# Kernel optimization log

Hardware: AMD Instinct MI355X
Metric: run time of the kernel (lower is better)

Reference implementation:

```python
import jax, jax.numpy as jnp
import numpy as np

N, E, G = 100000, 1600000, 8
IN, H, OUT = 3, 64, 20


def setup_inputs() -> dict:
    key = jax.random.key(0)
    ks = jax.random.split(key, 24)
    def nrm(k, shape, scale=0.1):
        return jax.random.normal(k, shape, dtype=jnp.float32) * scale
    inp = {}
    inp["x"] = jax.random.normal(ks[0], (N, IN), dtype=jnp.float32)
    inp["edge_index"] = jax.random.randint(ks[1], (2, E), 0, N, dtype=jnp.int32)
    inp["batch"] = jnp.sort(jax.random.randint(ks[2], (N,), 0, G, dtype=jnp.int32))
    dims = [(IN, H), (H, H), (H, H)]  # 3 GATConv layers (initial + layers-1)
    for i, (di, do) in enumerate(dims):
        inp[f"W{i}"] = nrm(ks[3 + 4 * i], (di, do))
        inp[f"as{i}"] = nrm(ks[4 + 4 * i], (do,))
        inp[f"ad{i}"] = nrm(ks[5 + 4 * i], (do,))
        inp[f"b{i}"] = jnp.zeros((do,), jnp.float32)
    inp["vn_emb0"] = jnp.zeros((1, H), jnp.float32)  # constant-0 init per module
    inp["m1_w1"] = nrm(ks[15], (H, H)); inp["m1_b1"] = jnp.zeros((H,), jnp.float32)
    inp["m1_w2"] = nrm(ks[16], (H, H)); inp["m1_b2"] = jnp.zeros((H,), jnp.float32)
    inp["mf_w1"] = nrm(ks[17], (H, H)); inp["mf_b1"] = jnp.zeros((H,), jnp.float32)
    inp["mf_w2"] = nrm(ks[18], (H, OUT)); inp["mf_b2"] = jnp.zeros((OUT,), jnp.float32)
    inp["out_w"] = nrm(ks[19], (H, OUT)); inp["out_b"] = jnp.zeros((OUT,), jnp.float32)
    return inp


def _gat(x, src, dst, W, a_s, a_d, b):
    # PyG GATConv, 1 head: h = xW; e_ij = LeakyReLU_0.2(a_s.h_j + a_d.h_i);
    # alpha = softmax over incoming edges of each dst node; out_i = sum_j alpha_ij h_j + b
    h = x @ W                                                  # [N, H]
    lg = jax.nn.leaky_relu((h @ a_s)[src] + (h @ a_d)[dst], 0.2)  # [E+N]
    m = jax.ops.segment_max(lg, dst, num_segments=N)
    m = jnp.where(jnp.isfinite(m), m, 0.0)
    p = jnp.exp(lg - m[dst])
    denom = jax.ops.segment_sum(p, dst, num_segments=N)
    alpha = p / denom[dst]
    return jax.ops.segment_sum(alpha[:, None] * h[src], dst, num_segments=N) + b


def _forward(x, edge_index, batch, params):
    (W0, as0, ad0, b0, W1, as1, ad1, b1, W2, as2, ad2, b2,
     vn_emb0, m1_w1, m1_b1, m1_w2, m1_b2, mf_w1, mf_b1, mf_w2, mf_b2,
     out_w, out_b) = params
    loops = jnp.arange(N, dtype=edge_index.dtype)  # GATConv add_self_loops=True
    src = jnp.concatenate([edge_index[0], loops])
    dst = jnp.concatenate([edge_index[1], loops])
    act = lambda v: jax.nn.leaky_relu(v, 0.01)  # nn.LeakyReLU default slope
    h = act(_gat(x, src, dst, W0, as0, ad0, b0))
    h = act(_gat(h, src, dst, W1, as1, ad1, b1))
    h = act(_gat(h, src, dst, W2, as2, ad2, b2))
    # virtual node: global_add_pool(out, batch) + Embedding(0) (zero-init)
    vn = jax.ops.segment_sum(h, batch, num_segments=G) + vn_emb0[0]
    vn = jax.nn.relu(vn @ m1_w1 + m1_b1)
    vn = jax.nn.relu(vn @ m1_w2 + m1_b2)
    vn = jax.nn.relu(vn @ mf_w1 + mf_b1)
    vn = jax.nn.relu(vn @ mf_w2 + mf_b2)
    return (h @ out_w + out_b, vn)


def reference(x, edge_index, batch, W0, as0, ad0, b0, W1, as1, ad1, b1,
              W2, as2, ad2, b2, vn_emb0, m1_w1, m1_b1, m1_w2, m1_b2,
              mf_w1, mf_b1, mf_w2, mf_b2, out_w, out_b):
    params = (W0, as0, ad0, b0, W1, as1, ad1, b1, W2, as2, ad2, b2,
              vn_emb0, m1_w1, m1_b1, m1_w2, m1_b2, mf_w1, mf_b1, mf_w2, mf_b2,
              out_w, out_b)
    return _forward(x, edge_index, batch, params)
```

## Files before the change

kernel.cpp:

```cpp
#include <hip/hip_runtime.h>
#include <hip/hip_bf16.h>

#define H 64
#define OUTD 20
#define NGRAPH 8
#define NBK 256
#define CAPB 8192
#define MAXDEG 63

typedef __attribute__((ext_vector_type(8))) short bf16x8;
typedef __attribute__((ext_vector_type(4))) float f32x4;
typedef __attribute__((ext_vector_type(8))) unsigned short u16x8;


__device__ __forceinline__ float ldp(const void* p, int i, bool f32) {
    return f32 ? ((const float*)p)[i]
               : __bfloat162float(((const __hip_bfloat16*)p)[i]);
}

__device__ __forceinline__ float bfu(unsigned short u) {
    union { unsigned int i; float f; } c; c.i = ((unsigned)u) << 16; return c.f;
}
__device__ __forceinline__ unsigned short fbits(float f) {
    __hip_bfloat16 b = __float2bfloat16(f);
    return *reinterpret_cast<unsigned short*>(&b);
}

__global__ void detect_dtype(const unsigned short* __restrict__ xb, int n_u16,
                             int* __restrict__ flag) {
    __shared__ int sh[256];
    int t = threadIdx.x;
    int m = min(n_u16, 4096);
    int bad = 0;
    for (int i = t; i < m; i += 256) {
        unsigned e = (xb[i] >> 7) & 0xFF;
        bad += (e >= 0x90) ? 1 : 0;
    }
    sh[t] = bad;
    __syncthreads();
    for (int off = 128; off; off >>= 1) {
        if (t < off) sh[t] += sh[t + off];
        __syncthreads();
    }
    if (t == 0) *flag = (sh[0] > (m >> 4)) ? 1 : 0;
}

__device__ __forceinline__ void ew_node(const float* __restrict__ s, float di,
                                        unsigned* __restrict__ cb,
                                        int deg, int node, int n, int l) {
    int D = deg + 1;
    int dm1 = deg;
    int e0 = l, e1 = l + 16, e2 = l + 32, e3 = l + 48;
    unsigned p0 = cb[min(e0, dm1)];
    unsigned p1 = cb[min(e1, dm1)];
    unsigned p2 = cb[min(e2, dm1)];
    unsigned p3 = cb[min(e3, dm1)];
    int j0 = (e0 < deg) ? (int)(p0 >> 15) : node;
    int j1 = (e1 < deg) ? (int)(p1 >> 15) : node;
    int j2 = (e2 < deg) ? (int)(p2 >> 15) : node;
    int j3 = (e3 < deg) ? (int)(p3 >> 15) : node;
    if ((unsigned)j0 >= (unsigned)n) j0 = 0;
    if ((unsigned)j1 >= (unsigned)n) j1 = 0;
    if ((unsigned)j2 >= (unsigned)n) j2 = 0;
    if ((unsigned)j3 >= (unsigned)n) j3 = 0;
    float v0 = s[j0] + di, v1 = s[j1] + di, v2 = s[j2] + di, v3 = s[j3] + di;
    v0 = v0 > 0.f ? v0 : 0.2f * v0;
    v1 = v1 > 0.f ? v1 : 0.2f * v1;
    v2 = v2 > 0.f ? v2 : 0.2f * v2;
    v3 = v3 > 0.f ? v3 : 0.2f * v3;
    bool m0 = e0 < D, m1 = e1 < D, m2 = e2 < D, m3 = e3 < D;
    float a0 = m0 ? v0 : -INFINITY, a1 = m1 ? v1 : -INFINITY;
    float a2 = m2 ? v2 : -INFINITY, a3 = m3 ? v3 : -INFINITY;
    float mx = fmaxf(fmaxf(a0, a1), fmaxf(a2, a3));
    for (int o = 1; o < 16; o <<= 1) mx = fmaxf(mx, __shfl_xor(mx, o));
    float x0 = m0 ? __expf(v0 - mx) : 0.f;
    float x1 = m1 ? __expf(v1 - mx) : 0.f;
    float x2 = m2 ? __expf(v2 - mx) : 0.f;
    float x3 = m3 ? __expf(v3 - mx) : 0.f;
    float ws = x0 + x1 + x2 + x3;
    for (int o = 1; o < 16; o <<= 1) ws += __shfl_xor(ws, o);
    float inv = 1.f / fmaxf(ws, 1e-20f);
    if (m0) cb[e0] = ((unsigned)j0 << 15) |
                     (((__float_as_uint(x0 * inv) + 0x8000u) >> 16) & 0x7FFFu);
    if (m1) cb[e1] = ((unsigned)j1 << 15) |
                     (((__float_as_uint(x1 * inv) + 0x8000u) >> 16) & 0x7FFFu);
    if (m2) cb[e2] = ((unsigned)j2 << 15) |
                     (((__float_as_uint(x2 * inv) + 0x8000u) >> 16) & 0x7FFFu);
    if (m3) cb[e3] = ((unsigned)j3 << 15) |
                     (((__float_as_uint(x3 * inv) + 0x8000u) >> 16) & 0x7FFFu);
}

__global__ void fillC_dense0(const int* __restrict__ src, const int* __restrict__ dst,
                             int* __restrict__ gcur, unsigned* __restrict__ ebuf,
                             int E, int n, int nC, int EPC, int nbk,
                             const void* __restrict__ x, const void* __restrict__ W,
                             const void* __restrict__ a_s, const void* __restrict__ a_d,
                             __hip_bfloat16* __restrict__ h, float* __restrict__ s,
                             float* __restrict__ d, const int* __restrict__ flagp) {
    if ((int)blockIdx.x < nC) {
        __shared__ unsigned lcnt[NBK];
        __shared__ int lbase[NBK];
        int t = threadIdx.x;
        for (int i = t; i < NBK; i += 256) lcnt[i] = 0;
        __syncthreads();
        int base = blockIdx.x * (256 * EPC) + t;
        for (int i = 0; i < EPC; ++i) {
            int e = base + i * 256;
            if (e < E) {
                int dn = dst[e];
                if ((unsigned)dn < (unsigned)n) atomicAdd(&lcnt[dn >> 9], 1u);
            }
        }
        __syncthreads();
        for (int i = t; i < nbk; i += 256) {
            unsigned c = lcnt[i];
            lbase[i] = c ? atomicAdd(&gcur[i], (int)c) : 0;
            lcnt[i] = 0;
        }
        __syncthreads();
        for (int i = 0; i < EPC; ++i) {
            int e = base + i * 256;
            if (e < E) {
                int dn = dst[e];
                if ((unsigned)dn < (unsigned)n) {
                    int b = dn >> 9;
                    unsigned pos = (unsigned)lbase[b] + atomicAdd(&lcnt[b], 1u);
                    if (pos < CAPB)
                        ebuf[(size_t)b * CAPB + pos] =
                            ((unsigned)src[e] << 9) | (unsigned)(dn & 511);
                }
            }
        }
        return;
    }
    const bool f32 = (*flagp != 0);
    int idx = ((int)blockIdx.x - nC) * 256 + threadIdx.x;
    int node = idx >> 6;
    int f = idx & 63;
    if (node >= n) return;
    float acc = 0.f;
    for (int k = 0; k < 3; ++k)
        acc += ldp(x, node * 3 + k, f32) * ldp(W, k * H + f, f32);
    ((short*)h)[((size_t)(f >> 5) * n + node) * 32 + (f & 31)] = (short)fbits(acc);
    float sv = acc * ldp(a_s, f, f32);
    float dv = acc * ldp(a_d, f, f32);
    for (int off = 32; off; off >>= 1) {
        sv += __shfl_xor(sv, off);
        dv += __shfl_xor(dv, off);
    }
    if (f == 0) { s[node] = sv; d[node] = dv; }
}

__global__ __launch_bounds__(512) void bucketD(const unsigned* __restrict__ ebuf,
                                               const int* __restrict__ gcur,
                                               unsigned* __restrict__ cntoff,
                                               unsigned* __restrict__ col,
                                               int* __restrict__ gtot, int n,
                                               const float* __restrict__ s,
                                               const float* __restrict__ d) {
    __shared__ unsigned lcnt[512];
    __shared__ int loff[512];
    __shared__ int sc[512];
    __shared__ int sdeg[512];
    __shared__ int sbase;
    int b = blockIdx.x, t = threadIdx.x;
    lcnt[t] = 0;
    __syncthreads();
    int end = min(gcur[b], CAPB);
    const unsigned* reg = ebuf + (size_t)b * CAPB;
    for (int i = t; i < end; i += 512) atomicAdd(&lcnt[reg[i] & 511u], 1u);
    __syncthreads();
    int node = (b << 9) + t;
    int degc = (node < n) ? (int)min(lcnt[t], (unsigned)MAXDEG) : -1;
    int slots = degc + 1;
    sc[t] = slots;
    __syncthreads();
    for (int ofs = 1; ofs < 512; ofs <<= 1) {
        int v = (t >= ofs) ? sc[t - ofs] : 0;
        __syncthreads();
        sc[t] += v;
        __syncthreads();
    }
    if (t == 511) sbase = atomicAdd(gtot, sc[511]);
    __syncthreads();
    int myoff = sbase + sc[t] - slots;
    int dg = (degc > 0) ? degc : 0;
    loff[t] = myoff;
    sdeg[t] = dg;
    if (node < n) cntoff[node] = (unsigned)myoff | ((unsigned)dg << 24);
    lcnt[t] = 0;
    __syncthreads();
    for (int i = t; i < end; i += 512) {
        unsigned e = reg[i];
        int loc = (int)(e & 511u);
        unsigned pos = atomicAdd(&lcnt[loc], 1u);
        if ((int)pos < sdeg[loc])
            col[loff[loc] + pos] = (e >> 9) << 15;
    }
    __syncthreads();
    int l = t & 15;
    int base16 = t >> 4;
    for (int it = 0; it < 16; ++it) {
        int local = base16 + 32 * it;
        int nd = (b << 9) + local;
        if (nd < n)
            ew_node(s, d[nd], col + loff[local], sdeg[local], nd, n, l);
    }
}

__global__ void edge_weights(const float* __restrict__ s, const float* __restrict__ d,
                             const unsigned* __restrict__ cntoff,
                             unsigned* __restrict__ col, int n) {
    int node = ((int)blockIdx.x * 256 + (int)threadIdx.x) >> 4;
    if (node >= n) return;
    unsigned co = cntoff[node];
    ew_node(s, d[node], col + (co & 0xFFFFFFu), (int)(co >> 24), node, n,
            threadIdx.x & 15);
}

#define ACC8(w, hv) { \
    a[0] += w * bfu(hv[0]); a[1] += w * bfu(hv[1]); \
    a[2] += w * bfu(hv[2]); a[3] += w * bfu(hv[3]); \
    a[4] += w * bfu(hv[4]); a[5] += w * bfu(hv[5]); \
    a[6] += w * bfu(hv[6]); a[7] += w * bfu(hv[7]); }

__global__ void gat_agg_sliced(const short* __restrict__ hs,
                               const unsigned* __restrict__ cntoff,
                               const unsigned* __restrict__ col,
                               const void* __restrict__ bias,
                               short* __restrict__ outs, int n,
                               const int* __restrict__ flagp) {
    const bool f32 = (*flagp != 0);
    int shp = (int)blockIdx.x & 7;
    int fh = shp >> 2, nq = shp & 3;
    int qN = (n + 3) >> 2;
    int node = nq * qN + ((int)blockIdx.x >> 3) * 8 + ((int)threadIdx.x >> 5);
    int lim = min(n, (nq + 1) * qN);
    if (node >= lim) return;
    int l = threadIdx.x & 31;
    int c = l & 3, q = l >> 2;
    unsigned co = cntoff[node];
    int D = (int)(co >> 24) + 1;
    const unsigned* cb = col + (co & 0xFFFFFFu);
    const u16x8* h8 = (const u16x8*)hs + (size_t)fh * n * 4 + c;

    int dm1 = D - 1;
    unsigned pk0 = cb[min(q, dm1)];
    unsigned pk1 = cb[min(q + 8, dm1)];
    unsigned pk2 = cb[min(q + 16, dm1)];
    pk0 = (q < D) ? pk0 : 0u;
    pk1 = (q + 8 < D) ? pk1 : 0u;
    pk2 = (q + 16 < D) ? pk2 : 0u;

    float a[8] = {0.f, 0.f, 0.f, 0.f, 0.f, 0.f, 0.f, 0.f};
    {
        u16x8 hv0 = h8[(size_t)(pk0 >> 15) * 4];
        u16x8 hv1 = h8[(size_t)(pk1 >> 15) * 4];
        u16x8 hv2 = h8[(size_t)(pk2 >> 15) * 4];
        float w0 = __uint_as_float((pk0 & 0x7FFFu) << 16);
        float w1 = __uint_as_float((pk1 & 0x7FFFu) << 16);
        float w2 = __uint_as_float((pk2 & 0x7FFFu) << 16);
        ACC8(w0, hv0);
        ACC8(w1, hv1);
        ACC8(w2, hv2);
    }
    if (D > 24) {
        unsigned pk3 = cb[min(q + 24, dm1)];
        unsigned pk4 = cb[min(q + 32, dm1)];
        unsigned pk5 = cb[min(q + 40, dm1)];
        unsigned pk6 = cb[min(q + 48, dm1)];
        unsigned pk7 = cb[min(q + 56, dm1)];
        pk3 = (q + 24 < D) ? pk3 : 0u;
        pk4 = (q + 32 < D) ? pk4 : 0u;
        pk5 = (q + 40 < D) ? pk5 : 0u;
        pk6 = (q + 48 < D) ? pk6 : 0u;
        pk7 = (q + 56 < D) ? pk7 : 0u;
        u16x8 hv3 = h8[(size_t)(pk3 >> 15) * 4];
        u16x8 hv4 = h8[(size_t)(pk4 >> 15) * 4];
        u16x8 hv5 = h8[(size_t)(pk5 >> 15) * 4];
        u16x8 hv6 = h8[(size_t)(pk6 >> 15) * 4];
        u16x8 hv7 = h8[(size_t)(pk7 >> 15) * 4];
        float w3 = __uint_as_float((pk3 & 0x7FFFu) << 16);
        float w4 = __uint_as_float((pk4 & 0x7FFFu) << 16);
        float w5 = __uint_as_float((pk5 & 0x7FFFu) << 16);
        float w6 = __uint_as_float((pk6 & 0x7FFFu) << 16);
        float w7 = __uint_as_float((pk7 & 0x7FFFu) << 16);
        ACC8(w3, hv3);
        ACC8(w4, hv4);
        ACC8(w5, hv5);
        ACC8(w6, hv6);
        ACC8(w7, hv7);
    }
#pragma unroll
    for (int i = 0; i < 8; ++i) {
        a[i] += __shfl_xor(a[i], 4);
        a[i] += __shfl_xor(a[i], 8);
        a[i] += __shfl_xor(a[i], 16);
    }
    if (q == 0) {
        u16x8 ov;
        for (int i = 0; i < 8; ++i) {
            float o = a[i] + ldp(bias, fh * 32 + c * 8 + i, f32);
            o = o > 0.f ? o : 0.01f * o;
            ov[i] = fbits(o);
        }
        ((u16x8*)outs)[((size_t)fh * n + node) * 4 + c] = ov;
    }
}


__global__ __launch_bounds__(256) void denseN_mfma(
    const __hip_bfloat16* __restrict__ in,
    const void* __restrict__ W,
    const void* __restrict__ a_s, const void* __restrict__ a_d,
    __hip_bfloat16* __restrict__ h, float* __restrict__ s,
    float* __restrict__ d, int n, const int* __restrict__ flagp) {
    const bool f32 = (*flagp != 0);
    __shared__ short Wt[64 * 72];
    int t = threadIdx.x;
    for (int i = t; i < 4096; i += 256) {
        int k = i >> 6, nf = i & 63;
        Wt[nf * 72 + k] = (short)fbits(ldp(W, i, f32));
    }
    __syncthreads();

    int wid = t >> 6, lane = t & 63;
    int quad = lane >> 4, n16 = lane & 15;
    int nodeBase = blockIdx.x * 64 + wid * 16;
    int mrow = nodeBase + n16;
    int mclamp = min(mrow, n - 1);
    const short* inp = (const short*)in;
    bf16x8 a0 = *(const bf16x8*)(inp + (size_t)mclamp * 32 + quad * 8);
    bf16x8 a1 = *(const bf16x8*)(inp + ((size_t)n + mclamp) * 32 + quad * 8);

    float as_v[4], ad_v[4];
    for (int nt = 0; nt < 4; ++nt) {
        as_v[nt] = ldp(a_s, nt * 16 + n16, f32);
        ad_v[nt] = ldp(a_d, nt * 16 + n16, f32);
    }

    float sv[4] = {0.f, 0.f, 0.f, 0.f}, dv[4] = {0.f, 0.f, 0.f, 0.f};
    f32x4 accs[4];
    for (int nt = 0; nt < 4; ++nt) {
        const short* wrow = Wt + (nt * 16 + n16) * 72;
        bf16x8 b0 = *(const bf16x8*)(wrow + quad * 8);
        bf16x8 b1 = *(const bf16x8*)(wrow + 32 + quad * 8);
        f32x4 cacc = {0.f, 0.f, 0.f, 0.f};
        cacc = __builtin_amdgcn_mfma_f32_16x16x32_bf16(a0, b0, cacc, 0, 0, 0);
        cacc = __builtin_amdgcn_mfma_f32_16x16x32_bf16(a1, b1, cacc, 0, 0, 0);
        accs[nt] = cacc;
        for (int r = 0; r < 4; ++r) {
            sv[r] += cacc[r] * as_v[nt];
            dv[r] += cacc[r] * ad_v[nt];
        }
    }

    short* hb = (short*)h;
    for (int r = 0; r < 4; ++r) {
        int node = nodeBase + quad * 4 + r;
        if (node < n) {
            for (int nt = 0; nt < 4; ++nt) {
                int f = nt * 16 + n16;
                hb[((size_t)(f >> 5) * n + node) * 32 + (f & 31)] = (short)fbits(accs[nt][r]);
            }
        }
    }
    for (int r = 0; r < 4; ++r) {
        for (int mask = 1; mask < 16; mask <<= 1) {
            sv[r] += __shfl_xor(sv[r], mask);
            dv[r] += __shfl_xor(dv[r], mask);
        }
    }
    if (n16 == 0) {
        for (int r = 0; r < 4; ++r) {
            int node = nodeBase + quad * 4 + r;
            if (node < n) { s[node] = sv[r]; d[node] = dv[r]; }
        }
    }
}


__global__ __launch_bounds__(256) void proj_pool(
    const __hip_bfloat16* __restrict__ h,
    const void* __restrict__ W, const void* __restrict__ b,
    void* __restrict__ out, int n, const int* __restrict__ flagp,
    int projBlocks, const int* __restrict__ batch, float* __restrict__ vn) {
    const bool f32 = (*flagp != 0);
    if ((int)blockIdx.x < projBlocks) {
        __shared__ short Wt[32 * 72];
        int t = threadIdx.x;
        for (int i = t; i < 32 * 64; i += 256) {
            int o = i >> 6, k = i & 63;
            Wt[o * 72 + k] = (o < OUTD) ? (short)fbits(ldp(W, k * OUTD + o, f32)) : 0;
        }
        __syncthreads();

        int wid = t >> 6, lane = t & 63;
        int quad = lane >> 4, n16 = lane & 15;
        int nodeBase = blockIdx.x * 64 + wid * 16;
        int mclamp = min(nodeBase + n16, n - 1);
        const short* hsrc = (const short*)h;
        bf16x8 a0 = *(const bf16x8*)(hsrc + (size_t)mclamp * 32 + quad * 8);
        bf16x8 a1 = *(const bf16x8*)(hsrc + ((size_t)n + mclamp) * 32 + quad * 8);

        f32x4 acc0 = {0.f, 0.f, 0.f, 0.f}, acc1 = {0.f, 0.f, 0.f, 0.f};
        {
            const short* wrow = Wt + n16 * 72;
            bf16x8 b0 = *(const bf16x8*)(wrow + quad * 8);
            bf16x8 b1 = *(const bf16x8*)(wrow + 32 + quad * 8);
            acc0 = __builtin_amdgcn_mfma_f32_16x16x32_bf16(a0, b0, acc0, 0, 0, 0);
            acc0 = __builtin_amdgcn_mfma_f32_16x16x32_bf16(a1, b1, acc0, 0, 0, 0);
        }
        {
            const short* wrow = Wt + (16 + n16) * 72;
            bf16x8 b0 = *(const bf16x8*)(wrow + quad * 8);
            bf16x8 b1 = *(const bf16x8*)(wrow + 32 + quad * 8);
            acc1 = __builtin_amdgcn_mfma_f32_16x16x32_bf16(a0, b0, acc1, 0, 0, 0);
            acc1 = __builtin_amdgcn_mfma_f32_16x16x32_bf16(a1, b1, acc1, 0, 0, 0);
        }
        float bv0 = ldp(b, n16, f32);
        float bv1 = (n16 < OUTD - 16) ? ldp(b, 16 + n16, f32) : 0.f;
        for (int r = 0; r < 4; ++r) {
            int node = nodeBase + quad * 4 + r;
            if (node >= n) break;
            float o0 = acc0[r] + bv0;
            if (f32) ((float*)out)[node * OUTD + n16] = o0;
            else     ((__hip_bfloat16*)out)[node * OUTD + n16] = __float2bfloat16(o0);
            if (n16 < OUTD - 16) {
                float o1 = acc1[r] + bv1;
                if (f32) ((float*)out)[node * OUTD + 16 + n16] = o1;
                else     ((__hip_bfloat16*)out)[node * OUTD + 16 + n16] = __float2bfloat16(o1);
            }
        }
        return;
    }
    __shared__ float part[NGRAPH * H];
    int t = threadIdx.x;
    for (int i = t; i < NGRAPH * H; i += 256) part[i] = 0.f;
    __syncthreads();
    int pb = (int)blockIdx.x - projBlocks;
    int npb = gridDim.x - projBlocks;
    int wid = t >> 6, lane = t & 63;
    int gwave = pb * 4 + wid;
    int nwaves = npb * 4;
    int chunk = (n + nwaves - 1) / nwaves;
    int beg = gwave * chunk;
    int end = min(n, beg + chunk);
    if (beg < end) {
        const short* hb = (const short*)h + (size_t)(lane >> 5) * n * 32 + (lane & 31);
        float acc = 0.f;
        int cur = batch[beg];
        for (int i = beg; i < end; ++i) {
            int g = batch[i];
            if (g != cur) {
                if ((unsigned)cur < NGRAPH) atomicAdd(&part[cur * H + lane], acc);
                acc = 0.f;
                cur = g;
            }
            acc += bfu((unsigned short)hb[(size_t)i * 32]);
        }
        if ((unsigned)cur < NGRAPH) atomicAdd(&part[cur * H + lane], acc);
    }
    __syncthreads();
    for (int i = t; i < NGRAPH * H; i += 256) {
        float v = part[i];
        if (v != 0.f) atomicAdd(&vn[i], v);
    }
}


__global__ void vn_mlp(const float* __restrict__ vn, const void* __restrict__ emb,
                       const void* __restrict__ w1, const void* __restrict__ b1,
                       const void* __restrict__ w2, const void* __restrict__ b2,
                       const void* __restrict__ w3, const void* __restrict__ b3,
                       const void* __restrict__ w4, const void* __restrict__ b4,
                       void* __restrict__ out, int out1_off, const int* __restrict__ flagp) {
    const bool f32 = (*flagp != 0);
    __shared__ float A[NGRAPH * H], B[NGRAPH * H];
    int t = threadIdx.x;
    int g = t >> 6, f = t & 63;
    A[t] = vn[t] + ldp(emb, f, f32);
    __syncthreads();
    float acc = ldp(b1, f, f32);
    for (int k = 0; k < H; ++k) acc += A[g * H + k] * ldp(w1, k * H + f, f32);
    B[t] = fmaxf(acc, 0.f);
    __syncthreads();
    acc = ldp(b2, f, f32);
    for (int k = 0; k < H; ++k) acc += B[g * H + k] * ldp(w2, k * H + f, f32);
    A[t] = fmaxf(acc, 0.f);
    __syncthreads();
    acc = ldp(b3, f, f32);
    for (int k = 0; k < H; ++k) acc += A[g * H + k] * ldp(w3, k * H + f, f32);
    B[t] = fmaxf(acc, 0.f);
    __syncthreads();
    if (f < OUTD) {
        acc = ldp(b4, f, f32);
        for (int k = 0; k < H; ++k) acc += B[g * H + k] * ldp(w4, k * OUTD + f, f32);
        acc = fmaxf(acc, 0.f);
        int idx = out1_off + g * OUTD + f;
        if (f32) ((float*)out)[idx] = acc;
        else     ((__hip_bfloat16*)out)[idx] = __float2bfloat16(acc);
    }
}


extern "C" void kernel_launch(void* const* d_in, const int* in_sizes, int n_in,
                              void* d_out, int out_size, void* d_ws, size_t ws_size,
                              hipStream_t stream) {
    const void* x   = d_in[0];
    const int* ei   = (const int*)d_in[1];
    const int* batch= (const int*)d_in[2];
    const void* W0  = d_in[3];
    const void* as0 = d_in[4];
    const void* ad0 = d_in[5];
    const void* b0  = d_in[6];
    const void* W1  = d_in[7];
    const void* as1 = d_in[8];
    const void* ad1 = d_in[9];
    const void* b1  = d_in[10];
    const void* W2  = d_in[11];
    const void* as2 = d_in[12];
    const void* ad2 = d_in[13];
    const void* b2  = d_in[14];
    const void* vne = d_in[15];
    const void* m1w1 = d_in[16];
    const void* m1b1 = d_in[17];
    const void* m1w2 = d_in[18];
    const void* m1b2 = d_in[19];
    const void* mfw1 = d_in[20];
    const void* mfb1 = d_in[21];
    const void* mfw2 = d_in[22];
    const void* mfb2 = d_in[23];
    const void* outw = d_in[24];
    const void* outb = d_in[25];

    const int N = in_sizes[2];
    const int E = in_sizes[1] / 2;
    const int* srcp = ei;
    const int* dstp = ei + E;

    char* w = (char*)d_ws;
    auto alloc = [&](size_t bytes) -> void* {
        void* p = (void*)w;
        w += ((bytes + 255) / 256) * 256;
        return p;
    };
    int*   flag   = (int*)alloc(256);
    int*   gcur   = (int*)alloc((size_t)NBK * 4);
    int*   gtot   = (int*)alloc(256);
    unsigned* ebuf= (unsigned*)alloc((size_t)NBK * CAPB * 4);
    unsigned* cntoff = (unsigned*)alloc((size_t)N * 4);
    unsigned* col = (unsigned*)alloc(((size_t)E + N + 64) * 4);
    __hip_bfloat16* featA = (__hip_bfloat16*)alloc((size_t)N * H * 2);
    __hip_bfloat16* featB = (__hip_bfloat16*)alloc((size_t)N * H * 2);
    __hip_bfloat16* hbuf  = (__hip_bfloat16*)alloc((size_t)N * H * 2);
    float* sArr   = (float*)alloc((size_t)N * 4);
    float* dArr   = (float*)alloc((size_t)N * 4);
    float* vn     = (float*)alloc((size_t)NGRAPH * H * 4);

    const int nbN64 = (N * H + 255) / 256;
    const int nb64 = (N + 63) / 64;
    const int projBlocks = (N + 63) / 64;
    const int nbk = (N + 511) >> 9;
    const int ewBlocks = (N + 15) / 16;
    const int qN = (N + 3) >> 2;
    const int aggBlocks = 8 * ((qN + 7) / 8);
    int EPC = 32;
    int nC = (E + 256 * EPC - 1) / (256 * EPC);
    while (nC > 256) { EPC <<= 1; nC = (E + 256 * EPC - 1) / (256 * EPC); }

    detect_dtype<<<1, 256, 0, stream>>>((const unsigned short*)x, in_sizes[0], flag);

    hipMemsetAsync(gcur, 0, (size_t)NBK * 4, stream);
    hipMemsetAsync(gtot, 0, 4, stream);
    hipMemsetAsync(vn, 0, (size_t)NGRAPH * H * 4, stream);
    fillC_dense0<<<nC + nbN64, 256, 0, stream>>>(
        srcp, dstp, gcur, ebuf, E, N, nC, EPC, nbk,
        x, W0, as0, ad0, hbuf, sArr, dArr, flag);
    bucketD<<<nbk, 512, 0, stream>>>(ebuf, gcur, cntoff, col, gtot, N, sArr, dArr);

    gat_agg_sliced<<<aggBlocks, 256, 0, stream>>>((const short*)hbuf, cntoff, col,
                                                  b0, (short*)featA, N, flag);
    denseN_mfma<<<nb64, 256, 0, stream>>>(featA, W1, as1, ad1, hbuf, sArr, dArr, N, flag);
    edge_weights<<<ewBlocks, 256, 0, stream>>>(sArr, dArr, cntoff, col, N);
    gat_agg_sliced<<<aggBlocks, 256, 0, stream>>>((const short*)hbuf, cntoff, col,
                                                  b1, (short*)featB, N, flag);
    denseN_mfma<<<nb64, 256, 0, stream>>>(featB, W2, as2, ad2, hbuf, sArr, dArr, N, flag);
    edge_weights<<<ewBlocks, 256, 0, stream>>>(sArr, dArr, cntoff, col, N);
    gat_agg_sliced<<<aggBlocks, 256, 0, stream>>>((const short*)hbuf, cntoff, col,
                                                  b2, (short*)featA, N, flag);

    proj_pool<<<projBlocks + 512, 256, 0, stream>>>(featA, outw, outb, d_out, N, flag,
                                                    projBlocks, batch, vn);
    vn_mlp<<<1, 512, 0, stream>>>(vn, vne, m1w1, m1b1, m1w2, m1b2, mfw1, mfb1, mfw2, mfb2,
                                  d_out, N * OUTD, flag);
}
```

Measured before the change: 422.9 us.

## Fuse edge softmax into GAT aggregation and drop separate edge-weight passes

```diff
diff --git a/kernel.cpp b/kernel.cpp
--- a/kernel.cpp
+++ b/kernel.cpp
@@ -43,51 +43,6 @@
         __syncthreads();
     }
     if (t == 0) *flag = (sh[0] > (m >> 4)) ? 1 : 0;
-}
-
-__device__ __forceinline__ void ew_node(const float* __restrict__ s, float di,
-                                        unsigned* __restrict__ cb,
-                                        int deg, int node, int n, int l) {
-    int D = deg + 1;
-    int dm1 = deg;
-    int e0 = l, e1 = l + 16, e2 = l + 32, e3 = l + 48;
-    unsigned p0 = cb[min(e0, dm1)];
-    unsigned p1 = cb[min(e1, dm1)];
-    unsigned p2 = cb[min(e2, dm1)];
-    unsigned p3 = cb[min(e3, dm1)];
-    int j0 = (e0 < deg) ? (int)(p0 >> 15) : node;
-    int j1 = (e1 < deg) ? (int)(p1 >> 15) : node;
-    int j2 = (e2 < deg) ? (int)(p2 >> 15) : node;
-    int j3 = (e3 < deg) ? (int)(p3 >> 15) : node;
-    if ((unsigned)j0 >= (unsigned)n) j0 = 0;
-    if ((unsigned)j1 >= (unsigned)n) j1 = 0;
-    if ((unsigned)j2 >= (unsigned)n) j2 = 0;
-    if ((unsigned)j3 >= (unsigned)n) j3 = 0;
-    float v0 = s[j0] + di, v1 = s[j1] + di, v2 = s[j2] + di, v3 = s[j3] + di;
-    v0 = v0 > 0.f ? v0 : 0.2f * v0;
-    v1 = v1 > 0.f ? v1 : 0.2f * v1;
-    v2 = v2 > 0.f ? v2 : 0.2f * v2;
-    v3 = v3 > 0.f ? v3 : 0.2f * v3;
-    bool m0 = e0 < D, m1 = e1 < D, m2 = e2 < D, m3 = e3 < D;
-    float a0 = m0 ? v0 : -INFINITY, a1 = m1 ? v1 : -INFINITY;
-    float a2 = m2 ? v2 : -INFINITY, a3 = m3 ? v3 : -INFINITY;
-    float mx = fmaxf(fmaxf(a0, a1), fmaxf(a2, a3));
-    for (int o = 1; o < 16; o <<= 1) mx = fmaxf(mx, __shfl_xor(mx, o));
-    float x0 = m0 ? __expf(v0 - mx) : 0.f;
-    float x1 = m1 ? __expf(v1 - mx) : 0.f;
-    float x2 = m2 ? __expf(v2 - mx) : 0.f;
-    float x3 = m3 ? __expf(v3 - mx) : 0.f;
-    float ws = x0 + x1 + x2 + x3;
-    for (int o = 1; o < 16; o <<= 1) ws += __shfl_xor(ws, o);
-    float inv = 1.f / fmaxf(ws, 1e-20f);
-    if (m0) cb[e0] = ((unsigned)j0 << 15) |
-                     (((__float_as_uint(x0 * inv) + 0x8000u) >> 16) & 0x7FFFu);
-    if (m1) cb[e1] = ((unsigned)j1 << 15) |
-                     (((__float_as_uint(x1 * inv) + 0x8000u) >> 16) & 0x7FFFu);
-    if (m2) cb[e2] = ((unsigned)j2 << 15) |
-                     (((__float_as_uint(x2 * inv) + 0x8000u) >> 16) & 0x7FFFu);
-    if (m3) cb[e3] = ((unsigned)j3 << 15) |
-                     (((__float_as_uint(x3 * inv) + 0x8000u) >> 16) & 0x7FFFu);
 }
 
 __global__ void fillC_dense0(const int* __restrict__ src, const int* __restrict__ dst,
@@ -154,10 +109,8 @@
 __global__ __launch_bounds__(512) void bucketD(const unsigned* __restrict__ ebuf,
                                                const int* __restrict__ gcur,
                                                unsigned* __restrict__ cntoff,
-                                               unsigned* __restrict__ col,
-                                               int* __restrict__ gtot, int n,
-                                               const float* __restrict__ s,
-                                               const float* __restrict__ d) {
+                                               int* __restrict__ col,
+                                               int* __restrict__ gtot, int n) {
     __shared__ unsigned lcnt[512];
     __shared__ int loff[512];
     __shared__ int sc[512];
@@ -195,27 +148,8 @@
         int loc = (int)(e & 511u);
         unsigned pos = atomicAdd(&lcnt[loc], 1u);
         if ((int)pos < sdeg[loc])
-            col[loff[loc] + pos] = (e >> 9) << 15;
-    }
-    __syncthreads();
-    int l = t & 15;
-    int base16 = t >> 4;
-    for (int it = 0; it < 16; ++it) {
-        int local = base16 + 32 * it;
-        int nd = (b << 9) + local;
-        if (nd < n)
-            ew_node(s, d[nd], col + loff[local], sdeg[local], nd, n, l);
-    }
-}
-
-__global__ void edge_weights(const float* __restrict__ s, const float* __restrict__ d,
-                             const unsigned* __restrict__ cntoff,
-                             unsigned* __restrict__ col, int n) {
-    int node = ((int)blockIdx.x * 256 + (int)threadIdx.x) >> 4;
-    if (node >= n) return;
-    unsigned co = cntoff[node];
-    ew_node(s, d[node], col + (co & 0xFFFFFFu), (int)(co >> 24), node, n,
-            threadIdx.x & 15);
+            col[loff[loc] + pos] = (int)(e >> 9);
+    }
 }
 
 #define ACC8(w, hv) { \
@@ -225,8 +159,10 @@
     a[6] += w * bfu(hv[6]); a[7] += w * bfu(hv[7]); }
 
 __global__ void gat_agg_sliced(const short* __restrict__ hs,
+                               const float* __restrict__ s,
+                               const float* __restrict__ d,
                                const unsigned* __restrict__ cntoff,
-                               const unsigned* __restrict__ col,
+                               const int* __restrict__ col,
                                const void* __restrict__ bias,
                                short* __restrict__ outs, int n,
                                const int* __restrict__ flagp) {
@@ -240,57 +176,104 @@
     int l = threadIdx.x & 31;
     int c = l & 3, q = l >> 2;
     unsigned co = cntoff[node];
-    int D = (int)(co >> 24) + 1;
-    const unsigned* cb = col + (co & 0xFFFFFFu);
+    int deg = (int)(co >> 24);
+    int D = deg + 1;
+    const int* cb = col + (co & 0xFFFFFFu);
     const u16x8* h8 = (const u16x8*)hs + (size_t)fh * n * 4 + c;
-
-    int dm1 = D - 1;
-    unsigned pk0 = cb[min(q, dm1)];
-    unsigned pk1 = cb[min(q + 8, dm1)];
-    unsigned pk2 = cb[min(q + 16, dm1)];
-    pk0 = (q < D) ? pk0 : 0u;
-    pk1 = (q + 8 < D) ? pk1 : 0u;
-    pk2 = (q + 16 < D) ? pk2 : 0u;
+    float di = d[node];
+
+    int e0 = q, e1 = q + 8, e2 = q + 16;
+    int s0 = cb[min(e0, deg)];
+    int s1 = cb[min(e1, deg)];
+    int s2 = cb[min(e2, deg)];
+    s0 = (e0 < deg) ? s0 : node;
+    s1 = (e1 < deg) ? s1 : node;
+    s2 = (e2 < deg) ? s2 : node;
+    if ((unsigned)s0 >= (unsigned)n) s0 = 0;
+    if ((unsigned)s1 >= (unsigned)n) s1 = 0;
+    if ((unsigned)s2 >= (unsigned)n) s2 = 0;
+    float v0 = s[s0] + di, v1 = s[s1] + di, v2 = s[s2] + di;
+    u16x8 hv0 = h8[(size_t)s0 * 4];
+    u16x8 hv1 = h8[(size_t)s1 * 4];
+    u16x8 hv2 = h8[(size_t)s2 * 4];
+    v0 = v0 > 0.f ? v0 : 0.2f * v0;
+    v1 = v1 > 0.f ? v1 : 0.2f * v1;
+    v2 = v2 > 0.f ? v2 : 0.2f * v2;
+    float sv0 = (e0 < D) ? v0 : -INFINITY;
+    float sv1 = (e1 < D) ? v1 : -INFINITY;
+    float sv2 = (e2 < D) ? v2 : -INFINITY;
+
+    float sv3 = -INFINITY, sv4 = -INFINITY, sv5 = -INFINITY,
+          sv6 = -INFINITY, sv7 = -INFINITY;
+    u16x8 hv3 = {}, hv4 = {}, hv5 = {}, hv6 = {}, hv7 = {};
+    bool big = (D > 24);
+    if (big) {
+        int e3 = q + 24, e4 = q + 32, e5 = q + 40, e6 = q + 48, e7 = q + 56;
+        int s3 = cb[min(e3, deg)];
+        int s4 = cb[min(e4, deg)];
+        int s5 = cb[min(e5, deg)];
+        int s6 = cb[min(e6, deg)];
+        int s7 = cb[min(e7, deg)];
+        s3 = (e3 < deg) ? s3 : node;
+        s4 = (e4 < deg) ? s4 : node;
+        s5 = (e5 < deg) ? s5 : node;
+        s6 = (e6 < deg) ? s6 : node;
+        s7 = (e7 < deg) ? s7 : node;
+        if ((unsigned)s3 >= (unsigned)n) s3 = 0;
+        if ((unsigned)s4 >= (unsigned)n) s4 = 0;
+        if ((unsigned)s5 >= (unsigned)n) s5 = 0;
+        if ((unsigned)s6 >= (unsigned)n) s6 = 0;
+        if ((unsigned)s7 >= (unsigned)n) s7 = 0;
+        float w3 = s[s3] + di, w4 = s[s4] + di, w5 = s[s5] + di,
+              w6 = s[s6] + di, w7 = s[s7] + di;
+        hv3 = h8[(size_t)s3 * 4];
+        hv4 = h8[(size_t)s4 * 4];
+        hv5 = h8[(size_t)s5 * 4];
+        hv6 = h8[(size_t)s6 * 4];
+        hv7 = h8[(size_t)s7 * 4];
+        w3 = w3 > 0.f ? w3 : 0.2f * w3;
+        w4 = w4 > 0.f ? w4 : 0.2f * w4;
+        w5 = w5 > 0.f ? w5 : 0.2f * w5;
+        w6 = w6 > 0.f ? w6 : 0.2f * w6;
+        w7 = w7 > 0.f ? w7 : 0.2f * w7;
+        sv3 = (e3 < D) ? w3 : -INFINITY;
+        sv4 = (e4 < D) ? w4 : -INFINITY;
+        sv5 = (e5 < D) ? w5 : -INFINITY;
+        sv6 = (e6 < D) ? w6 : -INFINITY;
+        sv7 = (e7 < D) ? w7 : -INFINITY;
+    }
+
+    float mx = fmaxf(fmaxf(fmaxf(sv0, sv1), fmaxf(sv2, sv3)),
+                     fmaxf(fmaxf(sv4, sv5), fmaxf(sv6, sv7)));
+    mx = fmaxf(mx, __shfl_xor(mx, 4));
+    mx = fmaxf(mx, __shfl_xor(mx, 8));
+    mx = fmaxf(mx, __shfl_xor(mx, 16));
+
+    float w0 = __expf(sv0 - mx);
+    float w1 = __expf(sv1 - mx);
+    float w2 = __expf(sv2 - mx);
+    float wsum = w0 + w1 + w2;
 
     float a[8] = {0.f, 0.f, 0.f, 0.f, 0.f, 0.f, 0.f, 0.f};
-    {
-        u16x8 hv0 = h8[(size_t)(pk0 >> 15) * 4];
-        u16x8 hv1 = h8[(size_t)(pk1 >> 15) * 4];
-        u16x8 hv2 = h8[(size_t)(pk2 >> 15) * 4];
-        float w0 = __uint_as_float((pk0 & 0x7FFFu) << 16);
-        float w1 = __uint_as_float((pk1 & 0x7FFFu) << 16);
-        float w2 = __uint_as_float((pk2 & 0x7FFFu) << 16);
-        ACC8(w0, hv0);
-        ACC8(w1, hv1);
-        ACC8(w2, hv2);
-    }
-    if (D > 24) {
-        unsigned pk3 = cb[min(q + 24, dm1)];
-        unsigned pk4 = cb[min(q + 32, dm1)];
-        unsigned pk5 = cb[min(q + 40, dm1)];
-        unsigned pk6 = cb[min(q + 48, dm1)];
-        unsigned pk7 = cb[min(q + 56, dm1)];
-        pk3 = (q + 24 < D) ? pk3 : 0u;
-        pk4 = (q + 32 < D) ? pk4 : 0u;
-        pk5 = (q + 40 < D) ? pk5 : 0u;
-        pk6 = (q + 48 < D) ? pk6 : 0u;
-        pk7 = (q + 56 < D) ? pk7 : 0u;
-        u16x8 hv3 = h8[(size_t)(pk3 >> 15) * 4];
-        u16x8 hv4 = h8[(size_t)(pk4 >> 15) * 4];
-        u16x8 hv5 = h8[(size_t)(pk5 >> 15) * 4];
-        u16x8 hv6 = h8[(size_t)(pk6 >> 15) * 4];
-        u16x8 hv7 = h8[(size_t)(pk7 >> 15) * 4];
-        float w3 = __uint_as_float((pk3 & 0x7FFFu) << 16);
-        float w4 = __uint_as_float((pk4 & 0x7FFFu) << 16);
-        float w5 = __uint_as_float((pk5 & 0x7FFFu) << 16);
-        float w6 = __uint_as_float((pk6 & 0x7FFFu) << 16);
-        float w7 = __uint_as_float((pk7 & 0x7FFFu) << 16);
+    ACC8(w0, hv0);
+    ACC8(w1, hv1);
+    ACC8(w2, hv2);
+    if (big) {
+        float w3 = __expf(sv3 - mx);
+        float w4 = __expf(sv4 - mx);
+        float w5 = __expf(sv5 - mx);
+        float w6 = __expf(sv6 - mx);
+        float w7 = __expf(sv7 - mx);
+        wsum += w3 + w4 + w5 + w6 + w7;
         ACC8(w3, hv3);
         ACC8(w4, hv4);
         ACC8(w5, hv5);
         ACC8(w6, hv6);
         ACC8(w7, hv7);
     }
+    wsum += __shfl_xor(wsum, 4);
+    wsum += __shfl_xor(wsum, 8);
+    wsum += __shfl_xor(wsum, 16);
 #pragma unroll
     for (int i = 0; i < 8; ++i) {
         a[i] += __shfl_xor(a[i], 4);
@@ -298,9 +281,10 @@
         a[i] += __shfl_xor(a[i], 16);
     }
     if (q == 0) {
+        float inv = 1.f / fmaxf(wsum, 1e-20f);
         u16x8 ov;
         for (int i = 0; i < 8; ++i) {
-            float o = a[i] + ldp(bias, fh * 32 + c * 8 + i, f32);
+            float o = a[i] * inv + ldp(bias, fh * 32 + c * 8 + i, f32);
             o = o > 0.f ? o : 0.01f * o;
             ov[i] = fbits(o);
         }
@@ -550,7 +534,7 @@
     int*   gtot   = (int*)alloc(256);
     unsigned* ebuf= (unsigned*)alloc((size_t)NBK * CAPB * 4);
     unsigned* cntoff = (unsigned*)alloc((size_t)N * 4);
-    unsigned* col = (unsigned*)alloc(((size_t)E + N + 64) * 4);
+    int*   col    = (int*)alloc(((size_t)E + N + 64) * 4);
     __hip_bfloat16* featA = (__hip_bfloat16*)alloc((size_t)N * H * 2);
     __hip_bfloat16* featB = (__hip_bfloat16*)alloc((size_t)N * H * 2);
     __hip_bfloat16* hbuf  = (__hip_bfloat16*)alloc((size_t)N * H * 2);
@@ -562,12 +546,11 @@
     const int nb64 = (N + 63) / 64;
     const int projBlocks = (N + 63) / 64;
     const int nbk = (N + 511) >> 9;
-    const int ewBlocks = (N + 15) / 16;
     const int qN = (N + 3) >> 2;
     const int aggBlocks = 8 * ((qN + 7) / 8);
-    int EPC = 32;
+    int EPC = 8;
     int nC = (E + 256 * EPC - 1) / (256 * EPC);
-    while (nC > 256) { EPC <<= 1; nC = (E + 256 * EPC - 1) / (256 * EPC); }
+    while (nC > 1024) { EPC <<= 1; nC = (E + 256 * EPC - 1) / (256 * EPC); }
 
     detect_dtype<<<1, 256, 0, stream>>>((const unsigned short*)x, in_sizes[0], flag);
 
@@ -577,18 +560,16 @@
     fillC_dense0<<<nC + nbN64, 256, 0, stream>>>(
         srcp, dstp, gcur, ebuf, E, N, nC, EPC, nbk,
         x, W0, as0, ad0, hbuf, sArr, dArr, flag);
-    bucketD<<<nbk, 512, 0, stream>>>(ebuf, gcur, cntoff, col, gtot, N, sArr, dArr);
-
-    gat_agg_sliced<<<aggBlocks, 256, 0, stream>>>((const short*)hbuf, cntoff, col,
-                                                  b0, (short*)featA, N, flag);
+    bucketD<<<nbk, 512, 0, stream>>>(ebuf, gcur, cntoff, col, gtot, N);
+
+    gat_agg_sliced<<<aggBlocks, 256, 0, stream>>>((const short*)hbuf, sArr, dArr,
+                                                  cntoff, col, b0, (short*)featA, N, flag);
     denseN_mfma<<<nb64, 256, 0, stream>>>(featA, W1, as1, ad1, hbuf, sArr, dArr, N, flag);
-    edge_weights<<<ewBlocks, 256, 0, stream>>>(sArr, dArr, cntoff, col, N);
-    gat_agg_sliced<<<aggBlocks, 256, 0, stream>>>((const short*)hbuf, cntoff, col,
-                                                  b1, (short*)featB, N, flag);
+    gat_agg_sliced<<<aggBlocks, 256, 0, stream>>>((const short*)hbuf, sArr, dArr,
+                                                  cntoff, col, b1, (short*)featB, N, flag);
     denseN_mfma<<<nb64, 256, 0, stream>>>(featB, W2, as2, ad2, hbuf, sArr, dArr, N, flag);
-    edge_weights<<<ewBlocks, 256, 0, stream>>>(sArr, dArr, cntoff, col, N);
-    gat_agg_sliced<<<aggBlocks, 256, 0, stream>>>((const short*)hbuf, cntoff, col,
-                                                  b2, (short*)featA, N, flag);
+    gat_agg_sliced<<<aggBlocks, 256, 0, stream>>>((const short*)hbuf, sArr, dArr,
+                                                  cntoff, col, b2, (short*)featA, N, flag);
 
     proj_pool<<<projBlocks + 512, 256, 0, stream>>>(featA, outw, outb, d_out, N, flag,
                                                     projBlocks, batch, vn);
```

Result: no change. 425.5 us (+0.6%).
